# Optimization experiments

Measured on AMD Instinct MI355X. Metric: run time of the kernel, lower is better.

## Reference

```python
import jax, jax.numpy as jnp
import numpy as np

B, N, F = 1024, 64, 512
EPS = 1e-8
NEG = -1e12


def setup_inputs() -> dict:
    key = jax.random.key(0)
    k1, k2, k3, k4, k5 = jax.random.split(key, 5)
    h = jax.random.normal(k1, (B, N, F), dtype=jnp.float32)
    # Linear weights stored as (in, out); math identical to torch x @ W.T
    W_h = jax.random.normal(k2, (F, F), dtype=jnp.float32) / np.sqrt(F)
    A_w1 = jax.random.normal(k3, (N, 4 * N), dtype=jnp.float32) / np.sqrt(N)
    A_w2 = jax.random.normal(k4, (4 * N, N), dtype=jnp.float32) / np.sqrt(4 * N)
    beta = jax.random.uniform(k5, (1,), dtype=jnp.float32)
    return {"h": h, "W_h": W_h, "beta": beta, "A_w1": A_w1, "A_w2": A_w2}


def _pearson_corr(x):
    # x: [B, N, F] -> pairwise Pearson correlation over feature dim: [B, N, N]
    xm = x - jnp.mean(x, axis=-1, keepdims=True)
    cov = jnp.einsum('bnf,bmf->bnm', xm, xm)          # [B, N, N]
    norm = jnp.sqrt(jnp.sum(xm * xm, axis=-1))        # [B, N]
    denom = norm[:, :, None] * norm[:, None, :] + EPS
    return cov / denom


def reference(h, W_h, beta, A_w1, A_w2):
    Wh = jnp.einsum('bnf,fg->bng', h, W_h)            # [B, N, F]
    corr_p = _pearson_corr(Wh)                        # [B, N, N]
    e = beta * jnp.abs(corr_p)                        # [B, N, N]
    # Adaptive graph structure learning: small MLP on last (node) dim
    hidden = jax.nn.relu(jnp.einsum('bnm,mk->bnk', e, A_w1))
    adj = jax.nn.relu(e + jnp.einsum('bnk,km->bnm', hidden, A_w2))
    attention = jnp.where(adj > 0, e, NEG)
    attention = jax.nn.softmax(attention, axis=-1)
    # dropout is identity in eval/reference mode
    h_prime = jnp.einsum('bnm,bmf->bnf', attention, Wh)
    return h_prime
```

## Files before the change

### kernel.cpp

```cpp
#include <hip/hip_runtime.h>
#include <math.h>

#define B_ 1024
#define N_ 64
#define F_ 512

typedef const __attribute__((address_space(1))) float* gptr_t;
typedef __attribute__((address_space(3))) float* lptr_t;
typedef _Float16 half_t;
typedef half_t half8 __attribute__((ext_vector_type(8)));
typedef half_t half4 __attribute__((ext_vector_type(4)));
typedef float f32x4 __attribute__((ext_vector_type(4)));

__device__ __forceinline__ void gload16(const float* g, float* l) {
  __builtin_amdgcn_global_load_lds((gptr_t)g, (lptr_t)l, 16, 0, 0);
}

#define XMI(n, f) ((n) * 128 + (((((f) >> 3) ^ ((n) >> 0 & 7))) << 3) + ((f) & 7))
#define SQI(n, m) ((n) * 64 + (((((m) >> 3) ^ ((n) & 7))) << 3) + ((m) & 7))

#define MFMA3(accv, ah, al, bh, bl)                                           \
  do {                                                                        \
    accv = __builtin_amdgcn_mfma_f32_16x16x32_f16(ah, bh, accv, 0, 0, 0);     \
    accv = __builtin_amdgcn_mfma_f32_16x16x32_f16(ah, bl, accv, 0, 0, 0);     \
    accv = __builtin_amdgcn_mfma_f32_16x16x32_f16(al, bh, accv, 0, 0, 0);     \
  } while (0)

__global__ __launch_bounds__(256) void k_split_w(const float* __restrict__ W,
                                                 half_t* __restrict__ wt_hi,
                                                 half_t* __restrict__ wt_lo) {
  int idx = blockIdx.x * 256 + threadIdx.x;
  int k = idx >> 9, n = idx & 511;
  float wv = W[idx] * 512.0f;
  half_t hh = (half_t)wv;
  half_t hl = (half_t)(wv - (float)hh);
  int f = (n ^ (n >> 1)) & 3;
  int pos = ((k >> 3) & 3) ^ f;
  int addr = n * 512 + (k & ~31) + (pos << 3) + (k & 7);
  wt_hi[addr] = hh;
  wt_lo[addr] = hl;
}

__global__ __launch_bounds__(256, 3) void k_wh(const float* __restrict__ hA,
                                               const half_t* __restrict__ WTh,
                                               const half_t* __restrict__ WTl,
                                               float* __restrict__ Wh) {
  __shared__ float  As[128 * 32];
  __shared__ half_t Bh[2][128 * 32];
  __shared__ half_t Bl[2][128 * 32];

  const int bid = blockIdx.x;
  const int wg  = (bid & 7) * 256 + (bid >> 3);
  const int mt  = wg >> 2;
  const int nt  = wg & 3;
  const int t = threadIdx.x;
  const int w = t >> 6, lane = t & 63;
  const int wr = w >> 1, wc = w & 1;
  const int lr = lane & 15, ko = lane >> 4;

  const float* Ab = hA + (size_t)mt * 128 * F_;
  const int n0 = nt * 128;

  int Asrc[4], Alds[4];
#pragma unroll
  for (int i = 0; i < 4; ++i) {
    int s = t + 256 * i;
    int row = s >> 3, j = s & 7;
    int jg = j ^ (row & 7);
    Asrc[i] = row * F_ + jg * 4;
    Alds[i] = s * 4;
  }
  int Bsrc[2], Blds[2];
#pragma unroll
  for (int i = 0; i < 2; ++i) {
    int s = t + 256 * i;
    int n = s >> 2, sl = s & 3;
    Bsrc[i] = (n0 + n) * 512 + sl * 8;
    Blds[i] = s * 8;
  }

  f32x4 acc[4][4];
#pragma unroll
  for (int i = 0; i < 4; ++i)
#pragma unroll
    for (int j = 0; j < 4; ++j) acc[i][j] = (f32x4){0.f, 0.f, 0.f, 0.f};

#define STAGE_A(k0)                                                          \
  do {                                                                       \
    _Pragma("unroll") for (int i_ = 0; i_ < 4; ++i_)                         \
        gload16(Ab + (size_t)(k0) + Asrc[i_], &As[Alds[i_]]);                \
  } while (0)

#define STAGE_B(buf, k0)                                                     \
  do {                                                                       \
    _Pragma("unroll") for (int i_ = 0; i_ < 2; ++i_)                         \
        gload16((const float*)(WTh + (size_t)(k0) + Bsrc[i_]),               \
                (float*)&Bh[buf][Blds[i_]]);                                 \
    _Pragma("unroll") for (int i_ = 0; i_ < 2; ++i_)                         \
        gload16((const float*)(WTl + (size_t)(k0) + Bsrc[i_]),               \
                (float*)&Bl[buf][Blds[i_]]);                                 \
  } while (0)

  STAGE_B(0, 0);
  STAGE_A(0);
  __syncthreads();

#pragma unroll 1
  for (int kt = 0; kt < 16; ++kt) {
    const int cur = kt & 1;
    if (kt < 15) STAGE_B(cur ^ 1, (kt + 1) * 32);

    half8 ah[4], al[4];
#pragma unroll
    for (int i = 0; i < 4; ++i) {
      int r = wr * 64 + i * 16 + lr;
      int p0 = (2 * ko) ^ (r & 7), p1 = (2 * ko + 1) ^ (r & 7);
      f32x4 x0 = *(const f32x4*)&As[r * 32 + p0 * 4];
      f32x4 x1 = *(const f32x4*)&As[r * 32 + p1 * 4];
#pragma unroll
      for (int q = 0; q < 4; ++q) {
        float xs = x0[q] * 16.0f;
        half_t hh = (half_t)xs;
        ah[i][q] = hh;
        al[i][q] = (half_t)(xs - (float)hh);
      }
#pragma unroll
      for (int q = 0; q < 4; ++q) {
        float xs = x1[q] * 16.0f;
        half_t hh = (half_t)xs;
        ah[i][4 + q] = hh;
        al[i][4 + q] = (half_t)(xs - (float)hh);
      }
    }

    __builtin_amdgcn_sched_barrier(0);
    __builtin_amdgcn_s_barrier();
    __builtin_amdgcn_sched_barrier(0);

    if (kt < 15) STAGE_A((kt + 1) * 32);

#pragma unroll
    for (int j = 0; j < 4; ++j) {
      int nb = wc * 64 + j * 16 + lr;
      int p = ko ^ ((nb ^ (nb >> 1)) & 3);
      half8 bh = *(const half8*)&Bh[cur][nb * 32 + p * 8];
      half8 bl = *(const half8*)&Bl[cur][nb * 32 + p * 8];
#pragma unroll
      for (int i = 0; i < 4; ++i) MFMA3(acc[i][j], ah[i], al[i], bh, bl);
    }

    __syncthreads();
  }

  const float sc = 1.0f / 8192.0f;
  float* whb = Wh + ((size_t)mt * 128 + wr * 64) * F_ + n0 + wc * 64;
#pragma unroll
  for (int i = 0; i < 4; ++i) {
#pragma unroll
    for (int rr = 0; rr < 4; ++rr) {
      int row = i * 16 + ko * 4 + rr;
#pragma unroll
      for (int j = 0; j < 4; ++j)
        whb[row * F_ + j * 16 + lr] = acc[i][j][rr] * sc;
    }
  }
#undef STAGE_A
#undef STAGE_B
}

__global__ __launch_bounds__(256) void k_attn(const float* __restrict__ Wh,
                                              const float* __restrict__ A1,
                                              const float* __restrict__ A2,
                                              const float* __restrict__ betap,
                                              float* __restrict__ out) {
  __shared__ float sm[12416];
  half_t* e_h   = (half_t*)sm;
  half_t* e_l   = e_h + 4096;
  half_t* xm_h  = (half_t*)(sm + 4096);
  half_t* xm_l  = xm_h + 8192;
  half_t* hid_h = (half_t*)(sm + 4096);
  half_t* hid_l = (half_t*)(sm + 6144);
  half_t* ab_h  = (half_t*)(sm + 8192);
  half_t* ab_l  = (half_t*)(sm + 10240);
  half_t* at_h  = (half_t*)sm;
  half_t* at_l  = at_h + 4096;
  half_t* wt_h  = (half_t*)(sm + 4096);
  half_t* wt_l  = (half_t*)(sm + 8192);
  float* mu  = sm + 12288;
  float* nrm = sm + 12352;

  const int b = blockIdx.x;
  const int t = threadIdx.x;
  const int w = t >> 6, lane = t & 63;
  const int lr = lane & 15, ko = lane >> 4;
  const float beta = betap[0];
  const float* whb = Wh + (size_t)b * N_ * F_;

  float4 vbuf[8];
#define LOAD_XM(c_)                                                           \
  do {                                                                        \
    _Pragma("unroll") for (int i_ = 0; i_ < 8; ++i_) {                        \
      int id_ = t + 256 * i_;                                                 \
      int n_ = id_ >> 5, c4_ = id_ & 31;                                      \
      vbuf[i_] = *(const float4*)(whb + n_ * F_ + (c_) * 128 + c4_ * 4);      \
    }                                                                         \
  } while (0)

  {
    int n = t >> 2, q = t & 3;
    const float* row = whb + n * F_ + q * 128;
    float s = 0.f;
#pragma unroll
    for (int i = 0; i < 32; ++i) {
      float4 v = *(const float4*)(row + i * 4);
      s += v.x + v.y + v.z + v.w;
    }
    s += __shfl_xor(s, 1);
    s += __shfl_xor(s, 2);
    if (q == 0) mu[n] = s * (1.f / F_);
  }
  LOAD_XM(0);
  __syncthreads();

  f32x4 covA[4];
#pragma unroll
  for (int j = 0; j < 4; ++j) covA[j] = (f32x4){0.f, 0.f, 0.f, 0.f};

#pragma unroll 1
  for (int c = 0; c < 4; ++c) {
#pragma unroll
    for (int i = 0; i < 8; ++i) {
      int id = t + 256 * i;
      int n = id >> 5, c4 = id & 31;
      float4 v = vbuf[i];
      float m_ = mu[n];
      float x0 = (v.x - m_) * 16.f, x1 = (v.y - m_) * 16.f;
      float x2 = (v.z - m_) * 16.f, x3 = (v.w - m_) * 16.f;
      half4 hh, hl;
      hh[0] = (half_t)x0; hl[0] = (half_t)(x0 - (float)hh[0]);
      hh[1] = (half_t)x1; hl[1] = (half_t)(x1 - (float)hh[1]);
      hh[2] = (half_t)x2; hl[2] = (half_t)(x2 - (float)hh[2]);
      hh[3] = (half_t)x3; hl[3] = (half_t)(x3 - (float)hh[3]);
      int ad = n * 128 + (((c4 >> 1) ^ (n & 7)) << 3) + (c4 & 1) * 4;
      *(half4*)&xm_h[ad] = hh;
      *(half4*)&xm_l[ad] = hl;
    }
    __syncthreads();
    if (c < 3) LOAD_XM(c + 1);
#pragma unroll
    for (int s = 0; s < 4; ++s) {
      int ra = w * 16 + lr;
      half8 ah = *(const half8*)&xm_h[XMI(ra, (s * 4 + ko) * 8)];
      half8 al = *(const half8*)&xm_l[XMI(ra, (s * 4 + ko) * 8)];
#pragma unroll
      for (int j = 0; j < 4; ++j) {
        int rb = j * 16 + lr;
        half8 bh = *(const half8*)&xm_h[XMI(rb, (s * 4 + ko) * 8)];
        half8 bl = *(const half8*)&xm_l[XMI(rb, (s * 4 + ko) * 8)];
        covA[j] = __builtin_amdgcn_mfma_f32_16x16x32_f16(ah, bh, covA[j], 0, 0, 0);
        covA[j] = __builtin_amdgcn_mfma_f32_16x16x32_f16(ah, bl, covA[j], 0, 0, 0);
        covA[j] = __builtin_amdgcn_mfma_f32_16x16x32_f16(al, bh, covA[j], 0, 0, 0);
      }
    }
    __syncthreads();
  }
#undef LOAD_XM

#pragma unroll
  for (int r = 0; r < 4; ++r)
    if (lr == 4 * ko + r) nrm[w * 16 + lr] = sqrtf(covA[w][r]);
  __syncthreads();

  float e32[4][4];
#pragma unroll
  for (int j = 0; j < 4; ++j) {
#pragma unroll
    for (int r = 0; r < 4; ++r) {
      int n = w * 16 + 4 * ko + r;
      int m = j * 16 + lr;
      float denom = nrm[n] * nrm[m] + 2.56e-6f;
      float e = beta * fabsf(covA[j][r] / denom);
      e32[j][r] = e;
      float es = e * 16.f;
      half_t hh = (half_t)es;
      e_h[SQI(n, m)] = hh;
      e_l[SQI(n, m)] = (half_t)(es - (float)hh);
    }
  }

  float a1buf[16], a2buf[16];
#define LOAD_A1(jc_)                                                          \
  do {                                                                        \
    _Pragma("unroll") for (int hf_ = 0; hf_ < 2; ++hf_)                       \
      _Pragma("unroll") for (int q_ = 0; q_ < 8; ++q_)                        \
        a1buf[hf_ * 8 + q_] =                                                 \
            A1[(size_t)((w + 4 * hf_) * 8 + q_) * 256 + (jc_) * 64 + lane];   \
  } while (0)
#define LOAD_A2(jc_)                                                          \
  do {                                                                        \
    _Pragma("unroll") for (int hf_ = 0; hf_ < 2; ++hf_)                       \
      _Pragma("unroll") for (int q_ = 0; q_ < 8; ++q_)                        \
        a2buf[hf_ * 8 + q_] =                                                 \
            A2[(size_t)((jc_) * 64 + (w + 4 * hf_) * 8 + q_) * 64 + lane];    \
  } while (0)

  LOAD_A1(0);
  __syncthreads();

  f32x4 adj[4];
#pragma unroll
  for (int j = 0; j < 4; ++j) adj[j] = (f32x4){0.f, 0.f, 0.f, 0.f};

#pragma unroll 1
  for (int jc = 0; jc < 4; ++jc) {
#pragma unroll
    for (int hf = 0; hf < 2; ++hf) {
      int mo = w + 4 * hf;
      int jl = lane;
      half8 hh, hl;
#pragma unroll
      for (int q = 0; q < 8; ++q) {
        float x = a1buf[hf * 8 + q] * 64.f;
        half_t h = (half_t)x;
        hh[q] = h; hl[q] = (half_t)(x - (float)h);
      }
      int ad = jl * 64 + ((mo ^ (jl & 7)) << 3);
      *(half8*)&ab_h[ad] = hh;
      *(half8*)&ab_l[ad] = hl;
    }
    __syncthreads();
    LOAD_A2(jc);

    f32x4 h1[4];
#pragma unroll
    for (int j = 0; j < 4; ++j) h1[j] = (f32x4){0.f, 0.f, 0.f, 0.f};
#pragma unroll
    for (int s = 0; s < 2; ++s) {
      int ra = w * 16 + lr;
      half8 ah = *(const half8*)&e_h[SQI(ra, (s * 4 + ko) * 8)];
      half8 al = *(const half8*)&e_l[SQI(ra, (s * 4 + ko) * 8)];
#pragma unroll
      for (int jt = 0; jt < 4; ++jt) {
        int jl = jt * 16 + lr;
        half8 bh = *(const half8*)&ab_h[SQI(jl, (s * 4 + ko) * 8)];
        half8 bl = *(const half8*)&ab_l[SQI(jl, (s * 4 + ko) * 8)];
        h1[jt] = __builtin_amdgcn_mfma_f32_16x16x32_f16(ah, bh, h1[jt], 0, 0, 0);
        h1[jt] = __builtin_amdgcn_mfma_f32_16x16x32_f16(ah, bl, h1[jt], 0, 0, 0);
        h1[jt] = __builtin_amdgcn_mfma_f32_16x16x32_f16(al, bh, h1[jt], 0, 0, 0);
      }
    }
#pragma unroll
    for (int jt = 0; jt < 4; ++jt) {
#pragma unroll
      for (int r = 0; r < 4; ++r) {
        float x = fmaxf(h1[jt][r], 0.f);
        int n = w * 16 + 4 * ko + r;
        int jl = jt * 16 + lr;
        half_t hh = (half_t)x;
        hid_h[SQI(n, jl)] = hh;
        hid_l[SQI(n, jl)] = (half_t)(x - (float)hh);
      }
    }
    __syncthreads();

#pragma unroll
    for (int hf = 0; hf < 2; ++hf) {
      int ko2 = w + 4 * hf;
      int m = lane;
      half8 hh, hl;
#pragma unroll
      for (int q = 0; q < 8; ++q) {
        float x = a2buf[hf * 8 + q] * 64.f;
        half_t h = (half_t)x;
        hh[q] = h; hl[q] = (half_t)(x - (float)h);
      }
      int ad = m * 64 + ((ko2 ^ (m & 7)) << 3);
      *(half8*)&ab_h[ad] = hh;
      *(half8*)&ab_l[ad] = hl;
    }
    __syncthreads();
    if (jc < 3) LOAD_A1(jc + 1);

#pragma unroll
    for (int s = 0; s < 2; ++s) {
      int ra = w * 16 + lr;
      half8 ah = *(const half8*)&hid_h[SQI(ra, (s * 4 + ko) * 8)];
      half8 al = *(const half8*)&hid_l[SQI(ra, (s * 4 + ko) * 8)];
#pragma unroll
      for (int mt = 0; mt < 4; ++mt) {
        int m = mt * 16 + lr;
        half8 bh = *(const half8*)&ab_h[SQI(m, (s * 4 + ko) * 8)];
        half8 bl = *(const half8*)&ab_l[SQI(m, (s * 4 + ko) * 8)];
        adj[mt] = __builtin_amdgcn_mfma_f32_16x16x32_f16(ah, bh, adj[mt], 0, 0, 0);
        adj[mt] = __builtin_amdgcn_mfma_f32_16x16x32_f16(ah, bl, adj[mt], 0, 0, 0);
        adj[mt] = __builtin_amdgcn_mfma_f32_16x16x32_f16(al, bh, adj[mt], 0, 0, 0);
      }
    }
    __syncthreads();
  }
#undef LOAD_A1
#undef LOAD_A2

  {
    float p[4][4];
#pragma unroll
    for (int r = 0; r < 4; ++r) {
      float mx = -3.0e38f;
#pragma unroll
      for (int mt = 0; mt < 4; ++mt) {
        float pre = e32[mt][r] + adj[mt][r] * (1.f / 65536.f);
        p[mt][r] = (pre > 0.f) ? e32[mt][r] : -1e12f;
        mx = fmaxf(mx, p[mt][r]);
      }
      mx = fmaxf(mx, __shfl_xor(mx, 1));
      mx = fmaxf(mx, __shfl_xor(mx, 2));
      mx = fmaxf(mx, __shfl_xor(mx, 4));
      mx = fmaxf(mx, __shfl_xor(mx, 8));
      float ssum = 0.f;
#pragma unroll
      for (int mt = 0; mt < 4; ++mt) {
        p[mt][r] = expf(p[mt][r] - mx);
        ssum += p[mt][r];
      }
      ssum += __shfl_xor(ssum, 1);
      ssum += __shfl_xor(ssum, 2);
      ssum += __shfl_xor(ssum, 4);
      ssum += __shfl_xor(ssum, 8);
      float inv = 1.f / ssum;
      int n = w * 16 + 4 * ko + r;
#pragma unroll
      for (int mt = 0; mt < 4; ++mt) {
        float pv = p[mt][r] * inv;
        int m = mt * 16 + lr;
        half_t hh = (half_t)pv;
        at_h[SQI(n, m)] = hh;
        at_l[SQI(n, m)] = (half_t)(pv - (float)hh);
      }
    }
  }

  const int fl0 = t & 127;
  const int moB = t >> 7;
  float wbuf[32];
#define LOAD_WT(fc_)                                                          \
  do {                                                                        \
    _Pragma("unroll") for (int i_ = 0; i_ < 4; ++i_) {                        \
      int mo_ = moB + 2 * i_;                                                 \
      _Pragma("unroll") for (int q_ = 0; q_ < 8; ++q_)                        \
        wbuf[i_ * 8 + q_] =                                                   \
            whb[(size_t)(mo_ * 8 + q_) * F_ + (fc_) * 128 + fl0];             \
    }                                                                         \
  } while (0)

  LOAD_WT(0);
#pragma unroll 1
  for (int fc = 0; fc < 4; ++fc) {
    __syncthreads();
#pragma unroll
    for (int i = 0; i < 4; ++i) {
      int mo = moB + 2 * i;
      half8 hh, hl;
#pragma unroll
      for (int q = 0; q < 8; ++q) {
        float x = wbuf[i * 8 + q];
        half_t h = (half_t)x;
        hh[q] = h; hl[q] = (half_t)(x - (float)h);
      }
      int ad = fl0 * 64 + ((mo ^ (fl0 & 7)) << 3);
      *(half8*)&wt_h[ad] = hh;
      *(half8*)&wt_l[ad] = hl;
    }
    __syncthreads();
    if (fc < 3) LOAD_WT(fc + 1);

    half8 aah[2], aal[2];
#pragma unroll
    for (int s = 0; s < 2; ++s) {
      int n = w * 16 + lr;
      aah[s] = *(const half8*)&at_h[SQI(n, (s * 4 + ko) * 8)];
      aal[s] = *(const half8*)&at_l[SQI(n, (s * 4 + ko) * 8)];
    }
#pragma unroll
    for (int ft = 0; ft < 8; ++ft) {
      f32x4 po = (f32x4){0.f, 0.f, 0.f, 0.f};
#pragma unroll
      for (int s = 0; s < 2; ++s) {
        int fl = ft * 16 + lr;
        int ad = fl * 64 + (((((s * 4 + ko)) ^ (fl & 7))) << 3);
        half8 bh = *(const half8*)&wt_h[ad];
        half8 bl = *(const half8*)&wt_l[ad];
        po = __builtin_amdgcn_mfma_f32_16x16x32_f16(aah[s], bh, po, 0, 0, 0);
        po = __builtin_amdgcn_mfma_f32_16x16x32_f16(aah[s], bl, po, 0, 0, 0);
        po = __builtin_amdgcn_mfma_f32_16x16x32_f16(aal[s], bh, po, 0, 0, 0);
      }
      int fg = fc * 128 + ft * 16 + lr;
#pragma unroll
      for (int r = 0; r < 4; ++r) {
        int n = w * 16 + 4 * ko + r;
        out[(size_t)b * N_ * F_ + n * F_ + fg] = po[r];
      }
    }
  }
#undef LOAD_WT
}

extern "C" void kernel_launch(void* const* d_in, const int* in_sizes, int n_in,
                              void* d_out, int out_size, void* d_ws, size_t ws_size,
                              hipStream_t stream) {
  const float* h    = (const float*)d_in[0];
  const float* W    = (const float*)d_in[1];
  const float* beta = (const float*)d_in[2];
  const float* A1   = (const float*)d_in[3];
  const float* A2   = (const float*)d_in[4];
  float* out = (float*)d_out;
  float* Wh  = (float*)d_ws;

  half_t* wt_hi = (half_t*)d_out;
  half_t* wt_lo = wt_hi + 512 * 512;

  k_split_w<<<1024, 256, 0, stream>>>(W, wt_hi, wt_lo);
  k_wh<<<2048, 256, 0, stream>>>(h, wt_hi, wt_lo, Wh);
  k_attn<<<B_, 256, 0, stream>>>(Wh, A1, A2, beta, out);
}
```

Before: 222.4 us.

## Split A tile to fp16 hi/lo once when staging through registers

The A tile used to be copied as fp32 straight into LDS with global_load_lds, and each wave converted it to hi/lo fp16 halves after reading. Now A is prefetched into registers, converted once per element, and written to LDS as swizzled hi/lo half8 vectors. Waves then read ready half8 fragments without repeating the split. This removes duplicated conversion work (both column waves converted the same rows) but adds register pressure, VMEM-to-register latency and LDS store traffic.

```diff
diff --git a/kernel.cpp b/kernel.cpp
--- a/kernel.cpp
+++ b/kernel.cpp
@@ -45,7 +45,8 @@
                                                const half_t* __restrict__ WTh,
                                                const half_t* __restrict__ WTl,
                                                float* __restrict__ Wh) {
-  __shared__ float  As[128 * 32];
+  __shared__ half_t Ah[128 * 32];
+  __shared__ half_t Alo[128 * 32];
   __shared__ half_t Bh[2][128 * 32];
   __shared__ half_t Bl[2][128 * 32];
 
@@ -61,14 +62,14 @@
   const float* Ab = hA + (size_t)mt * 128 * F_;
   const int n0 = nt * 128;
 
-  int Asrc[4], Alds[4];
-#pragma unroll
-  for (int i = 0; i < 4; ++i) {
-    int s = t + 256 * i;
-    int row = s >> 3, j = s & 7;
-    int jg = j ^ (row & 7);
-    Asrc[i] = row * F_ + jg * 4;
-    Alds[i] = s * 4;
+  int Arow[2], Aoct[2], Aad[2];
+#pragma unroll
+  for (int i = 0; i < 2; ++i) {
+    int id = t + 256 * i;
+    int row = id >> 2, oct = id & 3;
+    Arow[i] = row;
+    Aoct[i] = oct;
+    Aad[i] = row * 32 + ((oct ^ ((row ^ (row >> 1)) & 3)) << 3);
   }
   int Bsrc[2], Blds[2];
 #pragma unroll
@@ -85,10 +86,34 @@
 #pragma unroll
     for (int j = 0; j < 4; ++j) acc[i][j] = (f32x4){0.f, 0.f, 0.f, 0.f};
 
-#define STAGE_A(k0)                                                          \
+  float4 areg[2][2];
+
+#define LOADA(k0)                                                            \
   do {                                                                       \
-    _Pragma("unroll") for (int i_ = 0; i_ < 4; ++i_)                         \
-        gload16(Ab + (size_t)(k0) + Asrc[i_], &As[Alds[i_]]);                \
+    _Pragma("unroll") for (int i_ = 0; i_ < 2; ++i_) {                       \
+      const float* p = Ab + (size_t)Arow[i_] * F_ + (k0) + Aoct[i_] * 8;     \
+      areg[i_][0] = *(const float4*)p;                                       \
+      areg[i_][1] = *(const float4*)(p + 4);                                 \
+    }                                                                        \
+  } while (0)
+
+#define WRITEA()                                                             \
+  do {                                                                       \
+    _Pragma("unroll") for (int i_ = 0; i_ < 2; ++i_) {                       \
+      half8 hh, hl;                                                          \
+      _Pragma("unroll") for (int q = 0; q < 4; ++q) {                        \
+        float xs = ((const float*)&areg[i_][0])[q] * 16.0f;                  \
+        half_t h = (half_t)xs;                                               \
+        hh[q] = h; hl[q] = (half_t)(xs - (float)h);                          \
+      }                                                                      \
+      _Pragma("unroll") for (int q = 0; q < 4; ++q) {                        \
+        float xs = ((const float*)&areg[i_][1])[q] * 16.0f;                  \
+        half_t h = (half_t)xs;                                               \
+        hh[4 + q] = h; hl[4 + q] = (half_t)(xs - (float)h);                  \
+      }                                                                      \
+      *(half8*)&Ah[Aad[i_]] = hh;                                            \
+      *(half8*)&Alo[Aad[i_]] = hl;                                           \
+    }                                                                        \
   } while (0)
 
 #define STAGE_B(buf, k0)                                                     \
@@ -101,43 +126,34 @@
                 (float*)&Bl[buf][Blds[i_]]);                                 \
   } while (0)
 
+  LOADA(0);
   STAGE_B(0, 0);
-  STAGE_A(0);
+  WRITEA();
   __syncthreads();
 
 #pragma unroll 1
   for (int kt = 0; kt < 16; ++kt) {
     const int cur = kt & 1;
-    if (kt < 15) STAGE_B(cur ^ 1, (kt + 1) * 32);
+    if (kt < 15) {
+      STAGE_B(cur ^ 1, (kt + 1) * 32);
+      LOADA((kt + 1) * 32);
+    }
 
     half8 ah[4], al[4];
 #pragma unroll
     for (int i = 0; i < 4; ++i) {
       int r = wr * 64 + i * 16 + lr;
-      int p0 = (2 * ko) ^ (r & 7), p1 = (2 * ko + 1) ^ (r & 7);
-      f32x4 x0 = *(const f32x4*)&As[r * 32 + p0 * 4];
-      f32x4 x1 = *(const f32x4*)&As[r * 32 + p1 * 4];
-#pragma unroll
-      for (int q = 0; q < 4; ++q) {
-        float xs = x0[q] * 16.0f;
-        half_t hh = (half_t)xs;
-        ah[i][q] = hh;
-        al[i][q] = (half_t)(xs - (float)hh);
-      }
-#pragma unroll
-      for (int q = 0; q < 4; ++q) {
-        float xs = x1[q] * 16.0f;
-        half_t hh = (half_t)xs;
-        ah[i][4 + q] = hh;
-        al[i][4 + q] = (half_t)(xs - (float)hh);
-      }
-    }
-
+      int pa = r * 32 + ((ko ^ ((r ^ (r >> 1)) & 3)) << 3);
+      ah[i] = *(const half8*)&Ah[pa];
+      al[i] = *(const half8*)&Alo[pa];
+    }
+
+    asm volatile("s_waitcnt lgkmcnt(0)" ::: "memory");
     __builtin_amdgcn_sched_barrier(0);
     __builtin_amdgcn_s_barrier();
     __builtin_amdgcn_sched_barrier(0);
 
-    if (kt < 15) STAGE_A((kt + 1) * 32);
+    if (kt < 15) WRITEA();
 
 #pragma unroll
     for (int j = 0; j < 4; ++j) {
@@ -164,7 +180,8 @@
         whb[row * F_ + j * 16 + lr] = acc[i][j][rr] * sc;
     }
   }
-#undef STAGE_A
+#undef LOADA
+#undef WRITEA
 #undef STAGE_B
 }
 
```

Result: no change. 225.2 us (+1.3%).
